# Optimization experiments

Measured on AMD Instinct MI355X. Metric: run time of the kernel, lower is better.

## Reference

```python
import jax, jax.numpy as jnp
import numpy as np

N_GROUPS = 32
N_HEADS = 16
EPS = 1e-5


def group_norm(x, w, b):
    # x: [B, C, T]
    B, C, T = x.shape
    xg = x.reshape(B, N_GROUPS, C // N_GROUPS, T)
    mu = xg.mean(axis=(2, 3), keepdims=True)
    var = xg.var(axis=(2, 3), keepdims=True)
    xn = ((xg - mu) * jax.lax.rsqrt(var + EPS)).reshape(B, C, T)
    return xn * w[None, :, None] + b[None, :, None]


def setup_inputs() -> dict:
    key = jax.random.key(0)
    ks = jax.random.split(key, 5)
    B, C, T = 4, 1024, 1024
    return {
        "x": jax.random.normal(ks[0], (B, C, T), jnp.float32),
        "norm_weight": jnp.ones((C,), jnp.float32),
        "norm_bias": jnp.zeros((C,), jnp.float32),
        "qkv_w": jax.random.normal(ks[1], (3 * C, C), jnp.float32) * 0.02,
        "qkv_b": jax.random.normal(ks[2], (3 * C,), jnp.float32) * 0.02,
        "proj_w": jax.random.normal(ks[3], (C, C), jnp.float32) * 0.02,
        "proj_b": jax.random.normal(ks[4], (C,), jnp.float32) * 0.02,
    }


def reference(x, norm_weight, norm_bias, qkv_w, qkv_b, proj_w, proj_b):
    B, C, T = x.shape
    H = N_HEADS
    ch = C // H
    # GroupNorm + 1x1 conv to QKV: [B, 3C, T]
    xn = group_norm(x, norm_weight, norm_bias)
    qkv = jnp.einsum('oc,bct->bot', qkv_w, xn) + qkv_b[None, :, None]
    # Legacy layout: [B, H*3*ch, T] -> [B, H, 3, ch, T]
    qkv = qkv.reshape(B, H, 3, ch, T)
    q, k, v = qkv[:, :, 0], qkv[:, :, 1], qkv[:, :, 2]
    scale = 1.0 / jnp.sqrt(jnp.sqrt(jnp.asarray(ch, x.dtype)))
    w = jnp.einsum('bhct,bhcs->bhts', q * scale, k * scale)
    w = jax.nn.softmax(w.astype(jnp.float32), axis=-1).astype(w.dtype)
    a = jnp.einsum('bhts,bhcs->bhct', w, v).reshape(B, C, T)
    h = jnp.einsum('oc,bct->bot', proj_w, a) + proj_b[None, :, None]
    return x + h
```

## Files before the change

### kernel.cpp

```cpp
#include <hip/hip_runtime.h>
#include <hip/hip_bf16.h>

typedef __bf16 bf16;
typedef bf16  bf16x4 __attribute__((ext_vector_type(4)));
typedef bf16  bf16x8 __attribute__((ext_vector_type(8)));
typedef float f32x4  __attribute__((ext_vector_type(4)));

union B8 { bf16x8 v; bf16 e[8]; };
union B4 { bf16x4 v; bf16 e[4]; };
union F4 { f32x4 v; float e[4]; };

#define GLOAD_LDS16(g, l)                                            \
  __builtin_amdgcn_global_load_lds(                                  \
      (const __attribute__((address_space(1))) void*)(g),            \
      (__attribute__((address_space(3))) void*)(l), 16, 0, 0)

#define SWZ(arr, R, c8) (*(const bf16x8*)&(arr)[(size_t)(R) * 64 + (((c8) ^ ((R) & 7)) << 3)])

__global__ __launch_bounds__(256) void conv_w_kernel(
    const float* __restrict__ qkvw, const float* __restrict__ qkvb,
    const float* __restrict__ pw,
    bf16* __restrict__ Wb, bf16* __restrict__ Pb, float* __restrict__ bs)
{
  const int row = blockIdx.x;
  const int tid = threadIdx.x;
  if (row < 3072) {
    const float s = ((row % 192) < 128) ? 0.42468158f : 1.0f;
    const float4 a = ((const float4*)(qkvw + (size_t)row * 1024))[tid];
    B4 o;
    o.e[0] = (bf16)(a.x * s); o.e[1] = (bf16)(a.y * s);
    o.e[2] = (bf16)(a.z * s); o.e[3] = (bf16)(a.w * s);
    ((bf16x4*)(Wb + (size_t)row * 1024))[tid] = o.v;
    if (tid == 0) bs[row] = qkvb[row] * s;
  } else {
    const int r = row - 3072;
    const float4 a = ((const float4*)(pw + (size_t)r * 1024))[tid];
    B4 o;
    o.e[0] = (bf16)a.x; o.e[1] = (bf16)a.y;
    o.e[2] = (bf16)a.z; o.e[3] = (bf16)a.w;
    ((bf16x4*)(Pb + (size_t)r * 1024))[tid] = o.v;
  }
}

__global__ __launch_bounds__(256) void gn_t_kernel(
    const float* __restrict__ x, const float* __restrict__ w,
    const float* __restrict__ bias, bf16* __restrict__ xnt)
{
  const int blk = blockIdx.x;
  const int b = blk >> 6, g = (blk >> 1) & 31, half = blk & 1;
  const float* xp = x + (size_t)(b * 1024 + g * 32) * 1024;
  const int tid = threadIdx.x;

  float s = 0.f, ss = 0.f;
  for (int ch = tid; ch < 4096; ch += 256) {
    const float4* p = (const float4*)(xp + (size_t)ch * 8);
    float4 u0 = p[0], u1 = p[1];
    s  += u0.x + u0.y + u0.z + u0.w + u1.x + u1.y + u1.z + u1.w;
    ss += u0.x*u0.x + u0.y*u0.y + u0.z*u0.z + u0.w*u0.w
        + u1.x*u1.x + u1.y*u1.y + u1.z*u1.z + u1.w*u1.w;
  }
  #pragma unroll
  for (int m = 1; m < 64; m <<= 1) { s += __shfl_xor(s, m); ss += __shfl_xor(ss, m); }

  __shared__ float red[8];
  __shared__ float stats[2];
  const int wave = tid >> 6, lane = tid & 63;
  if (lane == 0) { red[wave] = s; red[4 + wave] = ss; }
  __syncthreads();
  if (tid == 0) {
    float ts  = red[0] + red[1] + red[2] + red[3];
    float tss = red[4] + red[5] + red[6] + red[7];
    float mu  = ts * (1.f / 32768.f);
    float var = tss * (1.f / 32768.f) - mu * mu;
    stats[0] = mu;
    stats[1] = rsqrtf(var + 1e-5f);
  }
  __syncthreads();
  const float mu = stats[0], rs = stats[1];

  for (int ti = half * 2; ti < half * 2 + 2; ++ti) {
    const int t = ti * 256 + tid;
    B8 o[4];
    #pragma unroll
    for (int cc = 0; cc < 32; ++cc) {
      const float wt = w[g * 32 + cc] * rs;
      const float bsv = bias[g * 32 + cc];
      const float v = xp[(size_t)cc * 1024 + t];
      o[cc >> 3].e[cc & 7] = (bf16)((v - mu) * wt + bsv);
    }
    bf16* dst = xnt + (size_t)(b * 1024 + t) * 1024 + g * 32;
    #pragma unroll
    for (int j = 0; j < 4; ++j) *(bf16x8*)(dst + j * 8) = o[j].v;
  }
}

__global__ __launch_bounds__(512, 2) void gemm_qkv_kernel(
    const bf16* __restrict__ xnt, const bf16* __restrict__ Wb,
    const float* __restrict__ bs, bf16* __restrict__ qkT, bf16* __restrict__ vv)
{
  const int bid = blockIdx.x;
  const int swz = (bid & 7) * 32 + (bid >> 3);
  const int bxn = swz >> 4, bym = swz & 15;
  const int n0 = bxn * 192, m0 = bym * 256;
  const int head = bxn;

  __shared__ __align__(16) bf16 Al[2][256 * 64];
  __shared__ __align__(16) bf16 Bl[2][192 * 64];

  const int tid  = threadIdx.x;
  const int wave = tid >> 6, lane = tid & 63;
  const int quad = lane >> 4, l15 = lane & 15;
  const int wr = wave >> 2, wc = wave & 3;
  const int lrow = lane >> 3, lp = lane & 7;
  const int sc8 = (lp ^ lrow) << 3;

  #define STAGE(bufn, kt) do {                                                \
    _Pragma("unroll")                                                         \
    for (int c = 0; c < 4; ++c)                                               \
      GLOAD_LDS16(xnt + (size_t)(m0 + c * 64 + wave * 8 + lrow) * 1024 +      \
                      (size_t)(kt) * 64 + sc8,                                \
                  &Al[bufn][(c * 64 + wave * 8) * 64]);                       \
    _Pragma("unroll")                                                         \
    for (int c = 0; c < 3; ++c)                                               \
      GLOAD_LDS16(Wb + (size_t)(n0 + c * 64 + wave * 8 + lrow) * 1024 +       \
                      (size_t)(kt) * 64 + sc8,                                \
                  &Bl[bufn][(c * 64 + wave * 8) * 64]);                       \
  } while (0)

  F4 acc[8][3];
  #pragma unroll
  for (int i = 0; i < 8; ++i)
    #pragma unroll
    for (int j = 0; j < 3; ++j) acc[i][j].v = (f32x4){0.f, 0.f, 0.f, 0.f};

  STAGE(0, 0);
  __syncthreads();

  for (int t = 0; t < 16; ++t) {
    const int cb = t & 1;

    bf16x8 af[2][8], bfr[2][3];
    #pragma unroll
    for (int kk = 0; kk < 2; ++kk) {
      #pragma unroll
      for (int nt = 0; nt < 3; ++nt)
        bfr[kk][nt] = SWZ(Bl[cb], wc * 48 + nt * 16 + l15, kk * 4 + quad);
      #pragma unroll
      for (int mt = 0; mt < 8; ++mt)
        af[kk][mt] = SWZ(Al[cb], wr * 128 + mt * 16 + l15, kk * 4 + quad);
    }

    if (t + 1 < 16) STAGE(cb ^ 1, t + 1);

    #pragma unroll
    for (int kk = 0; kk < 2; ++kk)
      #pragma unroll
      for (int mt = 0; mt < 8; ++mt)
        #pragma unroll
        for (int nt = 0; nt < 3; ++nt)
          acc[mt][nt].v = __builtin_amdgcn_mfma_f32_16x16x32_bf16(
              af[kk][mt], bfr[kk][nt], acc[mt][nt].v, 0, 0, 0);

    __syncthreads();
  }
  #undef STAGE

  const int z  = m0 >> 10;
  const int tb = (m0 & 1023) + wr * 128;
  #pragma unroll
  for (int nt = 0; nt < 3; ++nt) {
    const int r192 = wc * 48 + nt * 16;
    const float bb = bs[n0 + r192 + l15];
    if (r192 < 128) {
      const int col = head * 128 + r192 + l15;
      #pragma unroll
      for (int mt = 0; mt < 8; ++mt)
        #pragma unroll
        for (int r = 0; r < 4; ++r) {
          const int m = m0 + wr * 128 + mt * 16 + quad * 4 + r;
          qkT[(size_t)m * 2048 + col] = (bf16)(acc[mt][nt].e[r] + bb);
        }
    } else {
      bf16* vrow = vv + ((size_t)z * 1024 + head * 64 + (r192 - 128) + l15) * 1024;
      #pragma unroll
      for (int mt = 0; mt < 8; ++mt) {
        B4 pk;
        #pragma unroll
        for (int r = 0; r < 4; ++r) pk.e[r] = (bf16)(acc[mt][nt].e[r] + bb);
        *(bf16x4*)&vrow[tb + mt * 16 + quad * 4] = pk.v;
      }
    }
  }
}

__global__ __launch_bounds__(512, 2) void gemm_proj_kernel(
    const bf16* __restrict__ Pb, const bf16* __restrict__ Bt,
    float* __restrict__ out, const float* __restrict__ bias,
    const float* __restrict__ resf)
{
  const int bid = blockIdx.x;
  const int swz = (bid & 7) * 32 + (bid >> 3);
  const int mp = swz & 7, np = swz >> 3;
  const int m0 = mp * 128;
  const int n0g = np * 128;

  __shared__ __align__(16) bf16 Al[2][128 * 64];
  __shared__ __align__(16) bf16 Bl[2][128 * 64];

  const int tid  = threadIdx.x;
  const int wave = tid >> 6, lane = tid & 63;
  const int quad = lane >> 4, l15 = lane & 15;
  const int wr = wave >> 2, wc = wave & 3;
  const int lrow = lane >> 3, lp = lane & 7;
  const int sc8 = (lp ^ lrow) << 3;

  #define STAGE(bufn, kt) do {                                                \
    _Pragma("unroll")                                                         \
    for (int c = 0; c < 2; ++c)                                               \
      GLOAD_LDS16(Pb + (size_t)(m0 + c * 64 + wave * 8 + lrow) * 1024 +       \
                      (size_t)(kt) * 64 + sc8,                                \
                  &Al[bufn][(c * 64 + wave * 8) * 64]);                       \
    _Pragma("unroll")                                                         \
    for (int c = 0; c < 2; ++c)                                               \
      GLOAD_LDS16(Bt + (size_t)(n0g + c * 64 + wave * 8 + lrow) * 1024 +      \
                      (size_t)(kt) * 64 + sc8,                                \
                  &Bl[bufn][(c * 64 + wave * 8) * 64]);                       \
  } while (0)

  F4 acc[4][2];
  #pragma unroll
  for (int i = 0; i < 4; ++i)
    #pragma unroll
    for (int j = 0; j < 2; ++j) acc[i][j].v = (f32x4){0.f, 0.f, 0.f, 0.f};

  STAGE(0, 0);
  __syncthreads();

  for (int t = 0; t < 16; ++t) {
    const int cb = t & 1;

    bf16x8 af[2][4], bfr[2][2];
    #pragma unroll
    for (int kk = 0; kk < 2; ++kk) {
      #pragma unroll
      for (int mt = 0; mt < 4; ++mt)
        af[kk][mt] = SWZ(Al[cb], wr * 64 + mt * 16 + l15, kk * 4 + quad);
      #pragma unroll
      for (int nt = 0; nt < 2; ++nt)
        bfr[kk][nt] = SWZ(Bl[cb], wc * 32 + nt * 16 + l15, kk * 4 + quad);
    }

    if (t + 1 < 16) STAGE(cb ^ 1, t + 1);

    #pragma unroll
    for (int kk = 0; kk < 2; ++kk)
      #pragma unroll
      for (int mt = 0; mt < 4; ++mt)
        #pragma unroll
        for (int nt = 0; nt < 2; ++nt)
          acc[mt][nt].v = __builtin_amdgcn_mfma_f32_16x16x32_bf16(
              af[kk][mt], bfr[kk][nt], acc[mt][nt].v, 0, 0, 0);

    __syncthreads();
  }
  #undef STAGE

  const int z  = n0g >> 10;
  const int nl = n0g & 1023;
  const size_t zoff = (size_t)z * 1024 * 1024;
  #pragma unroll
  for (int mt = 0; mt < 4; ++mt) {
    #pragma unroll
    for (int r = 0; r < 4; ++r) {
      const int m = m0 + wr * 64 + mt * 16 + quad * 4 + r;
      const float bb = bias[m];
      #pragma unroll
      for (int nt = 0; nt < 2; ++nt) {
        const int n = nl + wc * 32 + nt * 16 + l15;
        out[zoff + (size_t)m * 1024 + n] =
            acc[mt][nt].e[r] + bb + resf[zoff + (size_t)m * 1024 + n];
      }
    }
  }
}

__global__ __launch_bounds__(256) void attn_kernel(
    const bf16* __restrict__ qkTin, const bf16* __restrict__ vmat,
    bf16* __restrict__ aout)
{
  const int h = blockIdx.x, tt = blockIdx.y, z = blockIdx.z;
  const bf16* qk = qkTin + (size_t)z * 1024 * 2048;
  const bf16* vp = vmat + (size_t)z * 1024 * 1024 + (size_t)(h * 64) * 1024;
  aout += (size_t)z * 1024 * 1024;
  const int t0 = tt * 128;

  __shared__ __align__(16) bf16 qP[128 * 64];
  __shared__ __align__(16) bf16 kl[2][64 * 64];
  __shared__ __align__(16) bf16 vl[2][64 * 64];

  const int tid  = threadIdx.x;
  const int wave = tid >> 6, lane = tid & 63;
  const int quad = lane >> 4, l15 = lane & 15;
  const int lrow = lane >> 3, lp = lane & 7;

  #pragma unroll
  for (int c = 0; c < 4; ++c) {
    const int row = wave * 32 + c * 8 + lrow;
    const int c8  = lp ^ (row & 7);
    GLOAD_LDS16(qk + (size_t)(t0 + row) * 2048 + h * 128 + c8 * 8,
                &qP[(wave * 32 + c * 8) * 64]);
  }
  const int r0 = wave * 16 + lrow, r1 = wave * 16 + 8 + lrow;
  const int c80 = lp ^ (r0 & 7), c81 = lp ^ (r1 & 7);
  GLOAD_LDS16(qk + (size_t)r0 * 2048 + h * 128 + 64 + c80 * 8, &kl[0][(wave * 16) * 64]);
  GLOAD_LDS16(qk + (size_t)r1 * 2048 + h * 128 + 64 + c81 * 8, &kl[0][(wave * 16 + 8) * 64]);
  GLOAD_LDS16(vp + (size_t)r0 * 1024 + c80 * 8, &vl[0][(wave * 16) * 64]);
  GLOAD_LDS16(vp + (size_t)r1 * 1024 + c81 * 8, &vl[0][(wave * 16 + 8) * 64]);
  __syncthreads();

  bf16x8 bq0[2], bq1[2];
  int prow[2];
  #pragma unroll
  for (int b = 0; b < 2; ++b) {
    const int Rq = wave * 32 + b * 16 + l15;
    bq0[b] = SWZ(qP, Rq, quad);
    bq1[b] = SWZ(qP, Rq, quad + 4);
    prow[b] = Rq;
  }

  float l_i[2] = {0.f, 0.f};
  F4 oacc[2][4];
  #pragma unroll
  for (int b = 0; b < 2; ++b)
    #pragma unroll
    for (int ct = 0; ct < 4; ++ct) oacc[b][ct].v = (f32x4){0.f, 0.f, 0.f, 0.f};

  const int pq8 = (quad & 1) * 4;

  int buf = 0;
  for (int s0 = 0; s0 < 1024; s0 += 64) {
    if (s0 + 64 < 1024) {
      const int nb = buf ^ 1, sn = s0 + 64;
      GLOAD_LDS16(qk + (size_t)(sn + r0) * 2048 + h * 128 + 64 + c80 * 8,
                  &kl[nb][(wave * 16) * 64]);
      GLOAD_LDS16(qk + (size_t)(sn + r1) * 2048 + h * 128 + 64 + c81 * 8,
                  &kl[nb][(wave * 16 + 8) * 64]);
      GLOAD_LDS16(vp + (size_t)r0 * 1024 + sn + c80 * 8, &vl[nb][(wave * 16) * 64]);
      GLOAD_LDS16(vp + (size_t)r1 * 1024 + sn + c81 * 8, &vl[nb][(wave * 16 + 8) * 64]);
    }

    bf16x8 ak0[4], ak1[4], bv[2][4];
    #pragma unroll
    for (int st = 0; st < 4; ++st) {
      const int Rk = st * 16 + l15;
      ak0[st] = SWZ(kl[buf], Rk, quad);
      ak1[st] = SWZ(kl[buf], Rk, quad + 4);
    }
    #pragma unroll
    for (int ks = 0; ks < 2; ++ks)
      #pragma unroll
      for (int ct = 0; ct < 4; ++ct)
        bv[ks][ct] = SWZ(vl[buf], ct * 16 + l15, ks * 4 + quad);

    #pragma unroll
    for (int b = 0; b < 2; ++b) {
      F4 sacc[4];
      #pragma unroll
      for (int st = 0; st < 4; ++st) sacc[st].v = (f32x4){0.f, 0.f, 0.f, 0.f};
      #pragma unroll
      for (int st = 0; st < 4; ++st) {
        sacc[st].v = __builtin_amdgcn_mfma_f32_16x16x32_bf16(ak0[st], bq0[b], sacc[st].v, 0, 0, 0);
        sacc[st].v = __builtin_amdgcn_mfma_f32_16x16x32_bf16(ak1[st], bq1[b], sacc[st].v, 0, 0, 0);
      }

      bf16* const pbase = &qP[(size_t)prow[b] * 64];
      #pragma unroll
      for (int st = 0; st < 4; ++st) {
        B4 pk;
        #pragma unroll
        for (int r = 0; r < 4; ++r) {
          const float p = __builtin_amdgcn_exp2f(sacc[st].e[r]);
          l_i[b] += p;
          pk.e[r] = (bf16)p;
        }
        const int c8 = (st * 2 + (quad >> 1)) ^ (prow[b] & 7);
        *(bf16x4*)(pbase + (c8 << 3) + pq8) = pk.v;
      }

      #pragma unroll
      for (int ks = 0; ks < 2; ++ks) {
        const bf16x8 ap = SWZ(qP, prow[b], ks * 4 + quad);
        #pragma unroll
        for (int ct = 0; ct < 4; ++ct)
          oacc[b][ct].v = __builtin_amdgcn_mfma_f32_16x16x32_bf16(
              ap, bv[ks][ct], oacc[b][ct].v, 0, 0, 0);
      }
    }
    __syncthreads();
    buf ^= 1;
  }

  #pragma unroll
  for (int b = 0; b < 2; ++b) {
    float li = l_i[b];
    li += __shfl_xor(li, 16);
    li += __shfl_xor(li, 32);
    const float inv = 1.f / li;
    float iv[4];
    #pragma unroll
    for (int r = 0; r < 4; ++r) iv[r] = __shfl(inv, quad * 4 + r);
    #pragma unroll
    for (int r = 0; r < 4; ++r) {
      const int t = t0 + wave * 32 + b * 16 + quad * 4 + r;
      #pragma unroll
      for (int ct = 0; ct < 4; ++ct)
        aout[(size_t)t * 1024 + h * 64 + ct * 16 + l15] = (bf16)(oacc[b][ct].e[r] * iv[r]);
    }
  }
}

extern "C" void kernel_launch(void* const* d_in, const int* in_sizes, int n_in,
                              void* d_out, int out_size, void* d_ws, size_t ws_size,
                              hipStream_t stream)
{
  const float* x    = (const float*)d_in[0];
  const float* nw   = (const float*)d_in[1];
  const float* nb   = (const float*)d_in[2];
  const float* qkvw = (const float*)d_in[3];
  const float* qkvb = (const float*)d_in[4];
  const float* pw   = (const float*)d_in[5];
  const float* pb   = (const float*)d_in[6];
  float* out = (float*)d_out;

  const long M1 = 1024L * 1024L;
  bf16*  xnt = (bf16*)d_ws;
  bf16*  qkT = xnt + 4 * M1;
  bf16*  vv  = xnt + 12 * M1;
  bf16*  at  = xnt + 16 * M1;
  bf16*  Wb  = xnt + 20 * M1;
  bf16*  Pb  = xnt + 23 * M1;
  float* bs  = (float*)(xnt + 24 * M1);

  conv_w_kernel<<<dim3(4096), dim3(256), 0, stream>>>(qkvw, qkvb, pw, Wb, Pb, bs);
  gn_t_kernel<<<dim3(256), dim3(256), 0, stream>>>(x, nw, nb, xnt);
  gemm_qkv_kernel<<<dim3(256), dim3(512), 0, stream>>>(xnt, Wb, bs, qkT, vv);
  attn_kernel<<<dim3(16, 8, 4), dim3(256), 0, stream>>>(qkT, vv, at);
  gemm_proj_kernel<<<dim3(256), dim3(512), 0, stream>>>(Pb, at, out, pb, x);
}
```

Before: 180.9 us.

## Merge GN halves, widen proj GEMM K-tile, reorder attention LDS reads

The group-norm kernel now has one block per (batch, group) that covers all timesteps, so the statistics are no longer computed twice per group. The projection GEMM stages a 128-wide K slice per iteration, halving loop trips and barriers at the cost of doubling shared memory per block, which may reduce occupancy. In the attention kernel, the K/V fragments are read from LDS before the next tile's asynchronous loads are issued.

```diff
diff --git a/kernel.cpp b/kernel.cpp
--- a/kernel.cpp
+++ b/kernel.cpp
@@ -47,7 +47,7 @@
     const float* __restrict__ bias, bf16* __restrict__ xnt)
 {
   const int blk = blockIdx.x;
-  const int b = blk >> 6, g = (blk >> 1) & 31, half = blk & 1;
+  const int b = blk >> 5, g = blk & 31;
   const float* xp = x + (size_t)(b * 1024 + g * 32) * 1024;
   const int tid = threadIdx.x;
 
@@ -78,7 +78,7 @@
   __syncthreads();
   const float mu = stats[0], rs = stats[1];
 
-  for (int ti = half * 2; ti < half * 2 + 2; ++ti) {
+  for (int ti = 0; ti < 4; ++ti) {
     const int t = ti * 256 + tid;
     B8 o[4];
     #pragma unroll
@@ -204,8 +204,8 @@
   const int m0 = mp * 128;
   const int n0g = np * 128;
 
-  __shared__ __align__(16) bf16 Al[2][128 * 64];
-  __shared__ __align__(16) bf16 Bl[2][128 * 64];
+  __shared__ __align__(16) bf16 Al[2][2][128 * 64];
+  __shared__ __align__(16) bf16 Bl[2][2][128 * 64];
 
   const int tid  = threadIdx.x;
   const int wave = tid >> 6, lane = tid & 63;
@@ -216,15 +216,17 @@
 
   #define STAGE(bufn, kt) do {                                                \
     _Pragma("unroll")                                                         \
-    for (int c = 0; c < 2; ++c)                                               \
-      GLOAD_LDS16(Pb + (size_t)(m0 + c * 64 + wave * 8 + lrow) * 1024 +       \
-                      (size_t)(kt) * 64 + sc8,                                \
-                  &Al[bufn][(c * 64 + wave * 8) * 64]);                       \
-    _Pragma("unroll")                                                         \
-    for (int c = 0; c < 2; ++c)                                               \
-      GLOAD_LDS16(Bt + (size_t)(n0g + c * 64 + wave * 8 + lrow) * 1024 +      \
-                      (size_t)(kt) * 64 + sc8,                                \
-                  &Bl[bufn][(c * 64 + wave * 8) * 64]);                       \
+    for (int h = 0; h < 2; ++h) {                                             \
+      _Pragma("unroll")                                                       \
+      for (int c = 0; c < 2; ++c) {                                           \
+        GLOAD_LDS16(Pb + (size_t)(m0 + c * 64 + wave * 8 + lrow) * 1024 +     \
+                        (size_t)(kt) * 128 + h * 64 + sc8,                    \
+                    &Al[bufn][h][(c * 64 + wave * 8) * 64]);                  \
+        GLOAD_LDS16(Bt + (size_t)(n0g + c * 64 + wave * 8 + lrow) * 1024 +    \
+                        (size_t)(kt) * 128 + h * 64 + sc8,                    \
+                    &Bl[bufn][h][(c * 64 + wave * 8) * 64]);                  \
+      }                                                                       \
+    }                                                                         \
   } while (0)
 
   F4 acc[4][2];
@@ -236,30 +238,34 @@
   STAGE(0, 0);
   __syncthreads();
 
-  for (int t = 0; t < 16; ++t) {
+  for (int t = 0; t < 8; ++t) {
     const int cb = t & 1;
 
-    bf16x8 af[2][4], bfr[2][2];
-    #pragma unroll
-    for (int kk = 0; kk < 2; ++kk) {
-      #pragma unroll
-      for (int mt = 0; mt < 4; ++mt)
-        af[kk][mt] = SWZ(Al[cb], wr * 64 + mt * 16 + l15, kk * 4 + quad);
-      #pragma unroll
-      for (int nt = 0; nt < 2; ++nt)
-        bfr[kk][nt] = SWZ(Bl[cb], wc * 32 + nt * 16 + l15, kk * 4 + quad);
-    }
-
-    if (t + 1 < 16) STAGE(cb ^ 1, t + 1);
-
-    #pragma unroll
-    for (int kk = 0; kk < 2; ++kk)
-      #pragma unroll
-      for (int mt = 0; mt < 4; ++mt)
+    bf16x8 af[2][2][4], bfr[2][2][2];
+    #pragma unroll
+    for (int h = 0; h < 2; ++h)
+      #pragma unroll
+      for (int kk = 0; kk < 2; ++kk) {
+        #pragma unroll
+        for (int mt = 0; mt < 4; ++mt)
+          af[h][kk][mt] = SWZ(Al[cb][h], wr * 64 + mt * 16 + l15, kk * 4 + quad);
         #pragma unroll
         for (int nt = 0; nt < 2; ++nt)
-          acc[mt][nt].v = __builtin_amdgcn_mfma_f32_16x16x32_bf16(
-              af[kk][mt], bfr[kk][nt], acc[mt][nt].v, 0, 0, 0);
+          bfr[h][kk][nt] = SWZ(Bl[cb][h], wc * 32 + nt * 16 + l15, kk * 4 + quad);
+      }
+
+    if (t + 1 < 8) STAGE(cb ^ 1, t + 1);
+
+    #pragma unroll
+    for (int h = 0; h < 2; ++h)
+      #pragma unroll
+      for (int kk = 0; kk < 2; ++kk)
+        #pragma unroll
+        for (int mt = 0; mt < 4; ++mt)
+          #pragma unroll
+          for (int nt = 0; nt < 2; ++nt)
+            acc[mt][nt].v = __builtin_amdgcn_mfma_f32_16x16x32_bf16(
+                af[h][kk][mt], bfr[h][kk][nt], acc[mt][nt].v, 0, 0, 0);
 
     __syncthreads();
   }
@@ -339,6 +345,19 @@
 
   int buf = 0;
   for (int s0 = 0; s0 < 1024; s0 += 64) {
+    bf16x8 ak0[4], ak1[4], bv[2][4];
+    #pragma unroll
+    for (int st = 0; st < 4; ++st) {
+      const int Rk = st * 16 + l15;
+      ak0[st] = SWZ(kl[buf], Rk, quad);
+      ak1[st] = SWZ(kl[buf], Rk, quad + 4);
+    }
+    #pragma unroll
+    for (int ks = 0; ks < 2; ++ks)
+      #pragma unroll
+      for (int ct = 0; ct < 4; ++ct)
+        bv[ks][ct] = SWZ(vl[buf], ct * 16 + l15, ks * 4 + quad);
+
     if (s0 + 64 < 1024) {
       const int nb = buf ^ 1, sn = s0 + 64;
       GLOAD_LDS16(qk + (size_t)(sn + r0) * 2048 + h * 128 + 64 + c80 * 8,
@@ -349,19 +368,6 @@
       GLOAD_LDS16(vp + (size_t)r1 * 1024 + sn + c81 * 8, &vl[nb][(wave * 16 + 8) * 64]);
     }
 
-    bf16x8 ak0[4], ak1[4], bv[2][4];
-    #pragma unroll
-    for (int st = 0; st < 4; ++st) {
-      const int Rk = st * 16 + l15;
-      ak0[st] = SWZ(kl[buf], Rk, quad);
-      ak1[st] = SWZ(kl[buf], Rk, quad + 4);
-    }
-    #pragma unroll
-    for (int ks = 0; ks < 2; ++ks)
-      #pragma unroll
-      for (int ct = 0; ct < 4; ++ct)
-        bv[ks][ct] = SWZ(vl[buf], ct * 16 + l15, ks * 4 + quad);
-
     #pragma unroll
     for (int b = 0; b < 2; ++b) {
       F4 sacc[4];
@@ -442,7 +448,7 @@
   float* bs  = (float*)(xnt + 24 * M1);
 
   conv_w_kernel<<<dim3(4096), dim3(256), 0, stream>>>(qkvw, qkvb, pw, Wb, Pb, bs);
-  gn_t_kernel<<<dim3(256), dim3(256), 0, stream>>>(x, nw, nb, xnt);
+  gn_t_kernel<<<dim3(128), dim3(256), 0, stream>>>(x, nw, nb, xnt);
   gemm_qkv_kernel<<<dim3(256), dim3(512), 0, stream>>>(xnt, Wb, bs, qkT, vv);
   attn_kernel<<<dim3(16, 8, 4), dim3(256), 0, stream>>>(qkT, vv, at);
   gemm_proj_kernel<<<dim3(256), dim3(512), 0, stream>>>(Pb, at, out, pb, x);
```

Measured after the change: 176.0 us. -2.7%, faster.
